# Kernel optimization log

Measured on AMD Instinct MI355X. Metric: run time of the kernel, lower is better.

The kernel has to match this reference:

```python
import jax, jax.numpy as jnp
import numpy as np

N = 100_000       # nodes
E_RAND = 1_600_000
HID = 256         # hidden_channels
L = 4             # num_layers
HEADS = 8
BASES = 4
AGGS = 3          # ['sum','mean','max']
DH = HID // HEADS # 32
BF = DH * BASES   # 128, bases_lin output dim
NG = 5000         # num graphs
VOCAB = 128
NFEAT = 9
EPS = 1e-5


def setup_inputs() -> dict:
    key = jax.random.key(0)
    ks = jax.random.split(key, 16)
    x = jax.random.randint(ks[0], (N, NFEAT), 0, VOCAB, dtype=jnp.int32)
    src = jax.random.randint(ks[1], (E_RAND,), 0, N, dtype=jnp.int32)
    dst = jax.random.randint(ks[2], (E_RAND,), 0, N, dtype=jnp.int32)
    loop = jnp.arange(N, dtype=jnp.int32)          # EGConv add_self_loops=True
    edge_src = jnp.concatenate([src, loop])
    edge_dst = jnp.concatenate([dst, loop])
    batch = jnp.sort(jax.random.randint(ks[3], (N,), 0, NG, dtype=jnp.int32))
    s = lambda k, shape, sc: (jax.random.normal(k, shape, jnp.float32) * sc)
    emb = s(ks[4], (NFEAT, VOCAB, HID), 0.1)       # AtomEncoder tables
    basesW = s(ks[5], (L, HID, BF), HID ** -0.5)
    combW = s(ks[6], (L, HID, HEADS * BASES * AGGS), HID ** -0.5)
    combB = jnp.zeros((L, HEADS * BASES * AGGS), jnp.float32)
    convBias = jnp.zeros((L, HID), jnp.float32)
    bnG = jnp.ones((L, HID), jnp.float32)
    bnB = jnp.zeros((L, HID), jnp.float32)
    mlp_w1 = s(ks[7], (HID, HID // 2), HID ** -0.5)
    bn1_g = jnp.ones((HID // 2,), jnp.float32)
    bn1_b = jnp.zeros((HID // 2,), jnp.float32)
    mlp_w2 = s(ks[8], (HID // 2, HID // 4), (HID // 2) ** -0.5)
    bn2_g = jnp.ones((HID // 4,), jnp.float32)
    bn2_b = jnp.zeros((HID // 4,), jnp.float32)
    mlp_w3 = s(ks[9], (HID // 4, 1), (HID // 4) ** -0.5)
    mlp_b3 = jnp.zeros((1,), jnp.float32)
    return dict(x=x, edge_src=edge_src, edge_dst=edge_dst, batch=batch,
                emb=emb, basesW=basesW, combW=combW, combB=combB,
                convBias=convBias, bnG=bnG, bnB=bnB,
                mlp_w1=mlp_w1, bn1_g=bn1_g, bn1_b=bn1_b,
                mlp_w2=mlp_w2, bn2_g=bn2_g, bn2_b=bn2_b,
                mlp_w3=mlp_w3, mlp_b3=mlp_b3)


def _batchnorm(h, g, b):
    # training-mode BatchNorm1d: biased batch stats
    mu = h.mean(0)
    var = ((h - mu) ** 2).mean(0)
    return (h - mu) * jax.lax.rsqrt(var + EPS) * g + b


def _egconv(x, src, dst, W_b, W_c, b_c, bias):
    bases = x @ W_b                                    # [N, BF]
    w = (x @ W_c + b_c).reshape(N, HEADS, BASES * AGGS)
    msg = bases[src]                                   # [E, BF] gather
    agg_sum = jnp.zeros((N, BF), x.dtype).at[dst].add(msg)
    deg = jnp.zeros((N,), x.dtype).at[dst].add(1.0)
    agg_mean = agg_sum / jnp.maximum(deg, 1.0)[:, None]
    agg_max = jnp.full((N, BF), -jnp.inf, x.dtype).at[dst].max(msg)
    agg = jnp.stack([agg_sum, agg_mean, agg_max], 1)   # [N, A, BF]
    agg = agg.reshape(N, AGGS * BASES, DH)             # [N, A*B, DH]
    out = jnp.einsum('nhk,nkd->nhd', w, agg).reshape(N, HID)
    return out + bias


def reference(x, edge_src, edge_dst, batch, emb, basesW, combW, combB,
              convBias, bnG, bnB, mlp_w1, bn1_g, bn1_b, mlp_w2, bn2_g,
              bn2_b, mlp_w3, mlp_b3):
    # AtomEncoder: sum of per-feature embedding lookups
    h = jnp.take_along_axis(
        emb.transpose(1, 0, 2),                        # [VOCAB, NFEAT, HID]
        x.T[..., None], axis=0) if False else None
    feat = jnp.arange(NFEAT)
    xe = emb[feat[None, :], x, :].sum(1)               # [N, HID]
    h = xe
    for l in range(L):
        c = _egconv(h, edge_src, edge_dst, basesW[l], combW[l], combB[l],
                    convBias[l])
        c = jax.nn.relu(_batchnorm(c, bnG[l], bnB[l]))
        h = h + c                                      # residual
    # global mean pool over graphs
    gs = jax.ops.segment_sum(h, batch, num_segments=NG)
    cnt = jax.ops.segment_sum(jnp.ones((N, 1), h.dtype), batch,
                              num_segments=NG)
    g = gs / jnp.maximum(cnt, 1.0)
    # MLP head
    g = jax.nn.relu(_batchnorm(g @ mlp_w1, bn1_g, bn1_b))
    g = jax.nn.relu(_batchnorm(g @ mlp_w2, bn2_g, bn2_b))
    return g @ mlp_w3 + mlp_b3                         # [NG, 1]
```

## Files before the change

### kernel.cpp

```cpp
#include <hip/hip_runtime.h>
#include <hip/hip_bf16.h>

#define NNODES 100000
#define HIDC 256
#define NFEAT 9
#define VOCABS 128
#define BFD 128
#define NCOMB 96
#define NGR 5000
#define LAYERSN 4
#define EPSV 1e-5f
#define SCHUNK 1024
#define NPP 16
#define NTILES 14
#define AGGBLK 2048
#define PBL (NTILES * 8 * 64)
#define NBUK 32
#define BDIV 3125
#define SC2K 64

typedef __hip_bfloat16 bf16;
typedef __attribute__((ext_vector_type(8))) short sh8;
typedef __attribute__((ext_vector_type(4))) float fx4;

__device__ __forceinline__ float b2f(bf16 v) { return __bfloat162float(v); }
__device__ __forceinline__ bf16 f2b(float v) { return __float2bfloat16(v); }
__device__ __forceinline__ float ldf(const float* p) { return *p; }
__device__ __forceinline__ float ldf(const bf16* p) { return b2f(*p); }
__device__ __forceinline__ void stf(float* p, float v) { *p = v; }
__device__ __forceinline__ void stf(bf16* p, float v) { *p = f2b(v); }
__device__ __forceinline__ float2 ldf2(const float* p) { return *(const float2*)p; }
__device__ __forceinline__ float2 ldf2(const bf16* p) {
    unsigned u = *(const unsigned*)p;
    return make_float2(__uint_as_float(u << 16), __uint_as_float(u & 0xFFFF0000u));
}
__device__ __forceinline__ void stf2(float* p, float a, float b) {
    *(float2*)p = make_float2(a, b);
}
__device__ __forceinline__ void stf2(bf16* p, float a, float b);

__device__ __forceinline__ unsigned pack2bf(float a, float b) {
    unsigned ua = __float_as_uint(a), ub = __float_as_uint(b);
    ua = (ua + 0x7FFFu + ((ua >> 16) & 1u)) >> 16;
    ub = (ub + 0x7FFFu + ((ub >> 16) & 1u)) >> 16;
    return ua | (ub << 16);
}
__device__ __forceinline__ void stf2(bf16* p, float a, float b) {
    *(unsigned*)p = pack2bf(a, b);
}

__global__ __launch_bounds__(256) void k_sentinel(float* out, int n, float val) {
    int i = blockIdx.x * 256 + threadIdx.x;
    if (i < n) out[i] = val;
}

__global__ __launch_bounds__(256) void k_hist(const int* __restrict__ dst,
                                              int* __restrict__ counts, int E) {
    int e = blockIdx.x * 256 + threadIdx.x;
    if (e < E) atomicAdd(&counts[dst[e]], 1);
}

__global__ __launch_bounds__(256) void k_scansum(const int* __restrict__ counts,
                                                 int* __restrict__ btot, int n) {
    __shared__ int sh[256];
    int b = blockIdx.x, t = threadIdx.x;
    int base = b * SCHUNK;
    int s = 0;
#pragma unroll
    for (int k = 0; k < 4; ++k) {
        int i = base + t + k * 256;
        if (i < n) s += counts[i];
    }
    sh[t] = s;
    __syncthreads();
    for (int st = 128; st > 0; st >>= 1) {
        if (t < st) sh[t] += sh[t + st];
        __syncthreads();
    }
    if (t == 0) btot[b] = sh[0];
}

__global__ void k_scansmall(const int* __restrict__ btot, int* __restrict__ boff, int nb) {
    if (threadIdx.x == 0 && blockIdx.x == 0) {
        int a = 0;
        for (int i = 0; i < nb; ++i) { boff[i] = a; a += btot[i]; }
    }
}

__global__ __launch_bounds__(256) void k_scanapply(const int* __restrict__ counts,
                                                   const int* __restrict__ boff,
                                                   int* __restrict__ rowptr,
                                                   int* __restrict__ cursor, int n) {
    __shared__ int sh[256];
    int b = blockIdx.x, t = threadIdx.x;
    int base = b * SCHUNK + t * 4;
    int c0 = (base + 0 < n) ? counts[base + 0] : 0;
    int c1 = (base + 1 < n) ? counts[base + 1] : 0;
    int c2 = (base + 2 < n) ? counts[base + 2] : 0;
    int c3 = (base + 3 < n) ? counts[base + 3] : 0;
    int s0 = c0, s1 = s0 + c1, s2 = s1 + c2, s3 = s2 + c3;
    sh[t] = s3;
    __syncthreads();
    for (int st = 1; st < 256; st <<= 1) {
        int v = (t >= st) ? sh[t - st] : 0;
        __syncthreads();
        sh[t] += v;
        __syncthreads();
    }
    int excl = sh[t] - s3 + boff[b];
    if (base + 0 < n) { rowptr[base + 1] = excl + s0; cursor[base + 0] = excl; }
    if (base + 1 < n) { rowptr[base + 2] = excl + s1; cursor[base + 1] = excl + s0; }
    if (base + 2 < n) { rowptr[base + 3] = excl + s2; cursor[base + 2] = excl + s1; }
    if (base + 3 < n) { rowptr[base + 4] = excl + s3; cursor[base + 3] = excl + s2; }
    if (b == 0 && t == 0) rowptr[0] = 0;
}

__global__ void k_binit(const int* __restrict__ rowptr, int* __restrict__ gcur) {
    int b = threadIdx.x;
    if (b < NBUK) gcur[b] = rowptr[b * BDIV];
}

__global__ __launch_bounds__(256) void k_bucket(const int* __restrict__ src,
                                                const int* __restrict__ dst,
                                                int* __restrict__ gcur,
                                                uint2* __restrict__ ebuf, int E) {
    __shared__ int cnt[NBUK], base[NBUK], off[NBUK];
    int tid = threadIdx.x;
    if (tid < NBUK) { cnt[tid] = 0; off[tid] = 0; }
    __syncthreads();
    int d[4], s[4], bk[4];
    int e0 = blockIdx.x * 1024;
#pragma unroll
    for (int k = 0; k < 4; ++k) {
        int e = e0 + tid + k * 256;
        if (e < E) {
            d[k] = dst[e]; s[k] = src[e];
            bk[k] = d[k] / BDIV;
            atomicAdd(&cnt[bk[k]], 1);
        } else bk[k] = -1;
    }
    __syncthreads();
    if (tid < NBUK && cnt[tid] > 0) base[tid] = atomicAdd(&gcur[tid], cnt[tid]);
    __syncthreads();
#pragma unroll
    for (int k = 0; k < 4; ++k) {
        if (bk[k] >= 0) {
            int sl = base[bk[k]] + atomicAdd(&off[bk[k]], 1);
            ebuf[sl] = make_uint2((unsigned)d[k], (unsigned)s[k]);
        }
    }
}

__global__ __launch_bounds__(256) void k_scatter2(const uint2* __restrict__ ebuf,
                                                  const int* __restrict__ rowptr,
                                                  int* __restrict__ cursor,
                                                  int* __restrict__ csr) {
    int bk = blockIdx.x & (NBUK - 1);
    int chunk = blockIdx.x >> 5;
    int lo = rowptr[bk * BDIV];
    int nhi = (bk + 1) * BDIV; if (nhi > NNODES) nhi = NNODES;
    int hi = rowptr[nhi];
    for (int e = lo + chunk * 256 + threadIdx.x; e < hi; e += SC2K * 256) {
        uint2 p = ebuf[e];
        int pos = atomicAdd(&cursor[p.x], 1);
        csr[pos] = (int)p.y;
    }
}

__global__ __launch_bounds__(256) void k_packB4(const float* __restrict__ basesW,
                                                const float* __restrict__ combW,
                                                bf16* __restrict__ Bp4) {
    int tid = blockIdx.x * 256 + threadIdx.x;
    if (tid >= LAYERSN * PBL) return;
    int layer = tid / PBL;
    int rem = tid % PBL;
    int l = rem & 63;
    int q = (rem >> 6) & 7;
    int t = rem >> 9;
    int n = t * 16 + (l & 15);
    int k0 = q * 32 + (l >> 4) * 8;
    const float* Wb = basesW + (size_t)layer * HIDC * BFD;
    const float* Wc = combW + (size_t)layer * HIDC * NCOMB;
    short out[8];
#pragma unroll
    for (int i = 0; i < 8; ++i) {
        int k = k0 + i;
        float v = (n < BFD) ? Wb[k * BFD + n] : Wc[k * NCOMB + (n - BFD)];
        unsigned u = __float_as_uint(v);
        out[i] = (short)((u + 0x7FFFu + ((u >> 16) & 1u)) >> 16);
    }
    *(sh8*)(Bp4 + (size_t)tid * 8) = *(sh8*)out;
}

template <typename TH, typename TW, int MODE>
__global__ __launch_bounds__(256) void k_gemm_mfma(TH* __restrict__ h,
                                                   const bf16* __restrict__ Bp,
                                                   const float* __restrict__ cb,
                                                   bf16* __restrict__ bases,
                                                   TW* __restrict__ wco,
                                                   const bf16* __restrict__ convp,
                                                   const float* __restrict__ ss,
                                                   const int* __restrict__ x,
                                                   const float* __restrict__ emb) {
    __shared__ unsigned ldsA[8192];
    __shared__ int xsh[64 * NFEAT];
    int tid = threadIdx.x;
    size_t blk = blockIdx.x;
    if (MODE == 0) {
        for (int i = tid; i < 64 * NFEAT; i += 256) {
            int row = i / NFEAT;
            size_t rg = blk * 64 + row;
            xsh[i] = (rg < NNODES) ? x[rg * NFEAT + (i % NFEAT)] : 0;
        }
        __syncthreads();
    }
#pragma unroll 4
    for (int it = 0; it < 32; ++it) {
        int p = tid + it * 256;
        int row = p >> 7, cp = p & 127;
        size_t rg = blk * 64 + row;
        unsigned word = 0;
        if (rg < NNODES) {
            int c0 = cp * 2;
            float a0, a1;
            if (MODE == 0) {
                a0 = 0.f; a1 = 0.f;
#pragma unroll
                for (int f = 0; f < NFEAT; ++f) {
                    const float* ep = emb + ((size_t)(f * VOCABS + xsh[row * NFEAT + f])) * HIDC + c0;
                    float2 ev = *(const float2*)ep;
                    a0 += ev.x; a1 += ev.y;
                }
                stf2(&h[rg * HIDC + c0], a0, a1);
            } else {
                float2 hv = ldf2(&h[rg * HIDC + c0]);
                a0 = hv.x; a1 = hv.y;
                unsigned cu = *(const unsigned*)&convp[rg * HIDC + c0];
                float2 sc = *(const float2*)&ss[c0];
                float2 sb = *(const float2*)&ss[HIDC + c0];
                float v0 = __uint_as_float(cu << 16) * sc.x + sb.x;
                float v1 = __uint_as_float(cu & 0xFFFF0000u) * sc.y + sb.y;
                a0 += fmaxf(v0, 0.f);
                a1 += fmaxf(v1, 0.f);
                stf2(&h[rg * HIDC + c0], a0, a1);
            }
            word = pack2bf(a0, a1);
        }
        ldsA[(row * 128 + cp) ^ ((row & 7) << 2)] = word;
    }
    __syncthreads();
    int w = tid >> 6, l = tid & 63;
    int r = 16 * w + (l & 15);
    sh8 af[8];
    const char* lb = (const char*)ldsA;
#pragma unroll
    for (int q = 0; q < 8; ++q) {
        int byte = (r * 512 + q * 64 + (l >> 4) * 16) ^ ((r & 7) << 4);
        af[q] = *(const sh8*)(lb + byte);
    }
    fx4 acc[NTILES];
#pragma unroll
    for (int t = 0; t < NTILES; ++t) acc[t] = (fx4){0.f, 0.f, 0.f, 0.f};
    const sh8* bp8 = (const sh8*)Bp;
#pragma unroll
    for (int t = 0; t < NTILES; ++t) {
#pragma unroll
        for (int q = 0; q < 8; ++q) {
            acc[t] = __builtin_amdgcn_mfma_f32_16x16x32_bf16(
                af[q], bp8[(t * 8 + q) * 64 + l], acc[t], 0, 0, 0);
        }
    }
#pragma unroll
    for (int t = 0; t < NTILES; ++t) {
#pragma unroll
        for (int j = 0; j < 4; ++j) {
            int rl = 16 * w + (l >> 4) * 4 + j;
            size_t rg = blk * 64 + rl;
            if (rg >= NNODES) continue;
            if (t < 8) {
                int col = t * 16 + (l & 15);
                bases[rg * BFD + col] = f2b(acc[t][j]);
            } else {
                int col = (t - 8) * 16 + (l & 15);
                stf(&wco[rg * NCOMB + col], acc[t][j] + cb[col]);
            }
        }
    }
}

template <typename TW>
__global__ __launch_bounds__(256) void k_agg(const int* __restrict__ rowptr,
                                             const int* __restrict__ csr,
                                             const uint4* __restrict__ b4,
                                             const TW* __restrict__ wco,
                                             const float* __restrict__ bias,
                                             bf16* __restrict__ conv,
                                             float* __restrict__ partials) {
    __shared__ float agg[8][3][BFD];
    __shared__ float red[512];
    int tid = threadIdx.x;
    int g = tid >> 5, cl = tid & 31;
    int sub = cl >> 4;
    int ln16 = cl & 15;
    red[tid] = 0.f;
    red[tid + 256] = 0.f;
    __syncthreads();
    int hh = cl >> 2;
    int dbase = 8 * (cl & 3);
    float bb[8];
#pragma unroll
    for (int j = 0; j < 8; ++j) bb[j] = bias[8 * cl + j];
    float sts[8], sts2[8];
#pragma unroll
    for (int j = 0; j < 8; ++j) { sts[j] = 0.f; sts2[j] = 0.f; }
    for (int n = blockIdx.x * 8 + g; n < NNODES; n += AGGBLK * 8) {
        int r0 = rowptr[n], r1 = rowptr[n + 1];
        float s0 = 0.f, s1 = 0.f, s2 = 0.f, s3 = 0.f;
        float s4 = 0.f, s5 = 0.f, s6 = 0.f, s7 = 0.f;
        float m0 = -INFINITY, m1 = -INFINITY, m2 = -INFINITY, m3 = -INFINITY;
        float m4 = -INFINITY, m5 = -INFINITY, m6 = -INFINITY, m7 = -INFINITY;
        int e = r0;
#define ACCU4(v) { float f0 = __uint_as_float((v).x << 16);            \
                   float f1 = __uint_as_float((v).x & 0xFFFF0000u);    \
                   float f2 = __uint_as_float((v).y << 16);            \
                   float f3 = __uint_as_float((v).y & 0xFFFF0000u);    \
                   float f4 = __uint_as_float((v).z << 16);            \
                   float f5 = __uint_as_float((v).z & 0xFFFF0000u);    \
                   float f6 = __uint_as_float((v).w << 16);            \
                   float f7 = __uint_as_float((v).w & 0xFFFF0000u);    \
                   s0 += f0; s1 += f1; s2 += f2; s3 += f3;             \
                   s4 += f4; s5 += f5; s6 += f6; s7 += f7;             \
                   m0 = fmaxf(m0, f0); m1 = fmaxf(m1, f1);             \
                   m2 = fmaxf(m2, f2); m3 = fmaxf(m3, f3);             \
                   m4 = fmaxf(m4, f4); m5 = fmaxf(m5, f5);             \
                   m6 = fmaxf(m6, f6); m7 = fmaxf(m7, f7); }
        for (; e + 8 <= r1; e += 8) {
            int i0 = csr[e + 0 + sub], i1 = csr[e + 2 + sub];
            int i2 = csr[e + 4 + sub], i3 = csr[e + 6 + sub];
            uint4 v0 = b4[(size_t)i0 * 16 + ln16];
            uint4 v1 = b4[(size_t)i1 * 16 + ln16];
            uint4 v2 = b4[(size_t)i2 * 16 + ln16];
            uint4 v3 = b4[(size_t)i3 * 16 + ln16];
            ACCU4(v0) ACCU4(v1) ACCU4(v2) ACCU4(v3)
        }
        for (; e + 2 <= r1; e += 2) {
            uint4 v = b4[(size_t)csr[e + sub] * 16 + ln16];
            ACCU4(v)
        }
        if (e < r1 && sub == 0) {
            uint4 v = b4[(size_t)csr[e] * 16 + ln16];
            ACCU4(v)
        }
#undef ACCU4
        s0 += __shfl_xor(s0, 16); s1 += __shfl_xor(s1, 16);
        s2 += __shfl_xor(s2, 16); s3 += __shfl_xor(s3, 16);
        s4 += __shfl_xor(s4, 16); s5 += __shfl_xor(s5, 16);
        s6 += __shfl_xor(s6, 16); s7 += __shfl_xor(s7, 16);
        m0 = fmaxf(m0, __shfl_xor(m0, 16)); m1 = fmaxf(m1, __shfl_xor(m1, 16));
        m2 = fmaxf(m2, __shfl_xor(m2, 16)); m3 = fmaxf(m3, __shfl_xor(m3, 16));
        m4 = fmaxf(m4, __shfl_xor(m4, 16)); m5 = fmaxf(m5, __shfl_xor(m5, 16));
        m6 = fmaxf(m6, __shfl_xor(m6, 16)); m7 = fmaxf(m7, __shfl_xor(m7, 16));
        if (sub == 0) {
            float inv = 1.0f / (float)(r1 - r0);
            int cb2 = ln16 * 8;
            *(float4*)&agg[g][0][cb2]     = make_float4(s0, s1, s2, s3);
            *(float4*)&agg[g][0][cb2 + 4] = make_float4(s4, s5, s6, s7);
            *(float4*)&agg[g][1][cb2]     = make_float4(s0 * inv, s1 * inv, s2 * inv, s3 * inv);
            *(float4*)&agg[g][1][cb2 + 4] = make_float4(s4 * inv, s5 * inv, s6 * inv, s7 * inv);
            *(float4*)&agg[g][2][cb2]     = make_float4(m0, m1, m2, m3);
            *(float4*)&agg[g][2][cb2 + 4] = make_float4(m4, m5, m6, m7);
        }
        const TW* wp = &wco[(size_t)n * NCOMB + hh * 12];
        float wv[12];
#pragma unroll
        for (int k = 0; k < 12; ++k) wv[k] = ldf(&wp[k]);
        float o[8];
#pragma unroll
        for (int j = 0; j < 8; ++j) {
            int d = dbase + j;
            float a = 0.f;
#pragma unroll
            for (int b = 0; b < 4; ++b) {
                a += wv[b] * agg[g][0][b * 32 + d];
                a += wv[4 + b] * agg[g][1][b * 32 + d];
                a += wv[8 + b] * agg[g][2][b * 32 + d];
            }
            a += bb[j];
            o[j] = a;
            sts[j] += a;
            sts2[j] += a * a;
        }
        uint4 cv = make_uint4(pack2bf(o[0], o[1]), pack2bf(o[2], o[3]),
                              pack2bf(o[4], o[5]), pack2bf(o[6], o[7]));
        ((uint4*)conv)[(size_t)n * 32 + cl] = cv;
    }
#pragma unroll
    for (int j = 0; j < 8; ++j) {
        atomicAdd(&red[8 * cl + j], sts[j]);
        atomicAdd(&red[256 + 8 * cl + j], sts2[j]);
    }
    __syncthreads();
    partials[(size_t)blockIdx.x * 512 + tid] = red[tid];
    partials[(size_t)blockIdx.x * 512 + 256 + tid] = red[tid + 256];
}

__global__ __launch_bounds__(256) void k_redstats(const float* __restrict__ partials,
                                                  float* __restrict__ sums) {
    int g = blockIdx.x * 256 + threadIdx.x;
    int j = g & 511;
    int chunk = g >> 9;
    float s = 0.f;
    for (int pb = chunk * 256; pb < (chunk + 1) * 256; ++pb)
        s += partials[(size_t)pb * 512 + j];
    atomicAdd(&sums[j], s);
}

template <int C>
__global__ void k_bnfin(const float* __restrict__ sums, const float* __restrict__ g,
                        const float* __restrict__ b, float nrows, float* __restrict__ ss) {
    int c = threadIdx.x;
    float mu = sums[c] / nrows;
    float var = sums[C + c] / nrows - mu * mu;
    float rstd = rsqrtf(fmaxf(var, 0.f) + EPSV);
    float sc = rstd * g[c];
    ss[c] = sc;
    ss[C + c] = b[c] - mu * sc;
}

template <typename TH>
__global__ __launch_bounds__(256) void k_pool(const TH* __restrict__ h,
                                              const bf16* __restrict__ conv,
                                              const float* __restrict__ ss,
                                              const int* __restrict__ batch,
                                              float* __restrict__ gs,
                                              float* __restrict__ cnt) {
    int c = threadIdx.x;
    float sc = ss[c], sb = ss[HIDC + c];
    int n0 = blockIdx.x * NPP;
    int end = min(n0 + NPP, NNODES);
    float acc = 0.f, ccnt = 0.f;
    int cur = batch[n0];
    for (int n = n0; n < end; ++n) {
        int b = batch[n];
        if (b != cur) {
            atomicAdd(&gs[(size_t)cur * HIDC + c], acc);
            if (c == 0) atomicAdd(&cnt[cur], ccnt);
            acc = 0.f; ccnt = 0.f; cur = b;
        }
        float v = b2f(conv[(size_t)n * HIDC + c]) * sc + sb;
        acc += ldf(&h[(size_t)n * HIDC + c]) + fmaxf(v, 0.f);
        ccnt += 1.f;
    }
    atomicAdd(&gs[(size_t)cur * HIDC + c], acc);
    if (c == 0) atomicAdd(&cnt[cur], ccnt);
}

__global__ __launch_bounds__(256) void k_pooldiv(float* __restrict__ gs,
                                                 const float* __restrict__ cnt) {
    int i = blockIdx.x * 256 + threadIdx.x;
    if (i >= NGR * HIDC) return;
    int ng = i >> 8;
    gs[i] = gs[i] / fmaxf(cnt[ng], 1.0f);
}

template <int K, int C>
__global__ void k_rowgemm(const float* __restrict__ in, const float* __restrict__ W,
                          float* __restrict__ out) {
    int r = blockIdx.x;
    __shared__ float rs[K];
    for (int i = threadIdx.x; i < K; i += C) rs[i] = in[r * K + i];
    __syncthreads();
    int c = threadIdx.x;
    float acc = 0.f;
    for (int k = 0; k < K; ++k) acc += rs[k] * W[k * C + c];
    out[r * C + c] = acc;
}

template <int C>
__global__ void k_stats(const float* __restrict__ a, int rows, int rpb,
                        float* __restrict__ sums) {
    int c = threadIdx.x;
    int r0 = blockIdx.x * rpb;
    int r1 = min(r0 + rpb, rows);
    float s = 0.f, s2 = 0.f;
    for (int r = r0; r < r1; ++r) {
        float v = a[r * C + c];
        s += v;
        s2 += v * v;
    }
    atomicAdd(&sums[c], s);
    atomicAdd(&sums[C + c], s2);
}

template <int C>
__global__ void k_apply_relu(float* __restrict__ a, const float* __restrict__ ss, int rows) {
    int i = blockIdx.x * 256 + threadIdx.x;
    if (i >= rows * C) return;
    int c = i % C;
    float v = a[i] * ss[c] + ss[C + c];
    a[i] = fmaxf(v, 0.f);
}

__global__ __launch_bounds__(256) void k_final(const float* __restrict__ g2,
                                               const float* __restrict__ w3,
                                               const float* __restrict__ b3,
                                               float* __restrict__ out) {
    int r = blockIdx.x * 256 + threadIdx.x;
    if (r >= NGR) return;
    float acc = 0.f;
#pragma unroll
    for (int k = 0; k < 64; ++k) acc += g2[r * 64 + k] * w3[k];
    out[r] = acc + b3[0];
}

static inline size_t alignup(size_t v) { return (v + 255) & ~(size_t)255; }

template <typename TH, typename TW>
static size_t carve_need(int E) {
    size_t off = 0;
    off = alignup(off + (size_t)NNODES * HIDC * sizeof(TH));
    off = alignup(off + (size_t)NNODES * BFD * 2);
    off = alignup(off + (size_t)NNODES * NCOMB * sizeof(TW));
    off = alignup(off + (size_t)NNODES * HIDC * 2);
    off = alignup(off + (size_t)(NNODES + 1) * 4);
    off = alignup(off + (size_t)NNODES * 4);
    off = alignup(off + (size_t)E * 4);
    off = alignup(off + (size_t)E * 8);
    off = alignup(off + 2 * HIDC * 4);
    off = alignup(off + 2 * HIDC * 4);
    off = alignup(off + 256 * 4);
    off = alignup(off + 256 * 4);
    off = alignup(off + 256 * 4);
    off = alignup(off + (size_t)LAYERSN * PBL * 8 * 2);
    off = alignup(off + (size_t)AGGBLK * 512 * 4);
    return off;
}

template <typename TH, typename TW>
static void run_all(const int* x, const int* esrc, const int* edst, const int* batch,
                    const float* emb, const float* basesW, const float* combW,
                    const float* combB, const float* convB, const float* bnG,
                    const float* bnB, const float* w1, const float* bn1g,
                    const float* bn1b, const float* w2, const float* bn2g,
                    const float* bn2b, const float* w3, const float* b3, int E,
                    float* out, char* base, hipStream_t stream) {
    size_t off = 0;
    TH* h = (TH*)(base + off);       off = alignup(off + (size_t)NNODES * HIDC * sizeof(TH));
    bf16* bases = (bf16*)(base + off); off = alignup(off + (size_t)NNODES * BFD * 2);
    TW* wco = (TW*)(base + off);     off = alignup(off + (size_t)NNODES * NCOMB * sizeof(TW));
    bf16* conv = (bf16*)(base + off); off = alignup(off + (size_t)NNODES * HIDC * 2);
    int* rowptr = (int*)(base + off); off = alignup(off + (size_t)(NNODES + 1) * 4);
    int* cursor = (int*)(base + off); off = alignup(off + (size_t)NNODES * 4);
    int* csr = (int*)(base + off);    off = alignup(off + (size_t)E * 4);
    size_t o_ebuf = off;
    uint2* ebuf = (uint2*)(base + off); off = alignup(off + (size_t)E * 8);
    float* sums = (float*)(base + off); off = alignup(off + 2 * HIDC * 4);
    float* ss = (float*)(base + off);   off = alignup(off + 2 * HIDC * 4);
    int* btot = (int*)(base + off);     off = alignup(off + 256 * 4);
    int* boff = (int*)(base + off);     off = alignup(off + 256 * 4);
    int* gcur = (int*)(base + off);     off = alignup(off + 256 * 4);
    bf16* Bp4 = (bf16*)(base + off);    off = alignup(off + (size_t)LAYERSN * PBL * 8 * 2);
    float* partials = (float*)(base + off); off = alignup(off + (size_t)AGGBLK * 512 * 4);
    size_t po = o_ebuf;
    float* gs = (float*)(base + po);  po = alignup(po + (size_t)NGR * HIDC * 4);
    float* cnt = (float*)(base + po); po = alignup(po + (size_t)NGR * 4);
    float* r1 = (float*)(base + po);  po = alignup(po + (size_t)NGR * 128 * 4);
    float* r2 = (float*)(base + po);  po = alignup(po + (size_t)NGR * 64 * 4);

    const int NB = (NNODES + SCHUNK - 1) / SCHUNK;
    const int GEMMBLK = (NNODES + 63) / 64;

    k_packB4<<<(LAYERSN * PBL + 255) / 256, 256, 0, stream>>>(basesW, combW, Bp4);
    hipMemsetAsync(cursor, 0, (size_t)NNODES * 4, stream);
    k_hist<<<(E + 255) / 256, 256, 0, stream>>>(edst, cursor, E);
    k_scansum<<<NB, 256, 0, stream>>>(cursor, btot, NNODES);
    k_scansmall<<<1, 64, 0, stream>>>(btot, boff, NB);
    k_scanapply<<<NB, 256, 0, stream>>>(cursor, boff, rowptr, cursor, NNODES);
    k_binit<<<1, NBUK, 0, stream>>>(rowptr, gcur);
    k_bucket<<<(E + 1023) / 1024, 256, 0, stream>>>(esrc, edst, gcur, ebuf, E);
    k_scatter2<<<NBUK * SC2K, 256, 0, stream>>>(ebuf, rowptr, cursor, csr);

    for (int l = 0; l < LAYERSN; ++l) {
        hipMemsetAsync(sums, 0, 2 * HIDC * 4, stream);
        if (l == 0) {
            k_gemm_mfma<TH, TW, 0><<<GEMMBLK, 256, 0, stream>>>(
                h, Bp4, combB, bases, wco, nullptr, ss, x, emb);
        } else {
            k_gemm_mfma<TH, TW, 1><<<GEMMBLK, 256, 0, stream>>>(
                h, Bp4 + (size_t)l * PBL * 8, combB + (size_t)l * NCOMB, bases, wco,
                conv, ss, nullptr, nullptr);
        }
        k_agg<TW><<<AGGBLK, 256, 0, stream>>>(rowptr, csr, (const uint4*)bases,
                                              wco, convB + (size_t)l * HIDC, conv,
                                              partials);
        k_redstats<<<16, 256, 0, stream>>>(partials, sums);
        k_bnfin<HIDC><<<1, HIDC, 0, stream>>>(sums, bnG + (size_t)l * HIDC,
                                              bnB + (size_t)l * HIDC, (float)NNODES, ss);
    }

    hipMemsetAsync(gs, 0, (size_t)NGR * HIDC * 4, stream);
    hipMemsetAsync(cnt, 0, (size_t)NGR * 4, stream);
    k_pool<TH><<<(NNODES + NPP - 1) / NPP, 256, 0, stream>>>(h, conv, ss, batch, gs, cnt);
    k_pooldiv<<<(NGR * HIDC + 255) / 256, 256, 0, stream>>>(gs, cnt);

    k_rowgemm<256, 128><<<NGR, 128, 0, stream>>>(gs, w1, r1);
    hipMemsetAsync(sums, 0, 2 * 128 * 4, stream);
    k_stats<128><<<(NGR + 15) / 16, 128, 0, stream>>>(r1, NGR, 16, sums);
    k_bnfin<128><<<1, 128, 0, stream>>>(sums, bn1g, bn1b, (float)NGR, ss);
    k_apply_relu<128><<<(NGR * 128 + 255) / 256, 256, 0, stream>>>(r1, ss, NGR);

    k_rowgemm<128, 64><<<NGR, 64, 0, stream>>>(r1, w2, r2);
    hipMemsetAsync(sums, 0, 2 * 64 * 4, stream);
    k_stats<64><<<(NGR + 31) / 32, 64, 0, stream>>>(r2, NGR, 32, sums);
    k_bnfin<64><<<1, 64, 0, stream>>>(sums, bn2g, bn2b, (float)NGR, ss);
    k_apply_relu<64><<<(NGR * 64 + 255) / 256, 256, 0, stream>>>(r2, ss, NGR);

    k_final<<<(NGR + 255) / 256, 256, 0, stream>>>(r2, w3, b3, out);
}

extern "C" void kernel_launch(void* const* d_in, const int* in_sizes, int n_in,
                              void* d_out, int out_size, void* d_ws, size_t ws_size,
                              hipStream_t stream) {
    const int* x        = (const int*)d_in[0];
    const int* esrc     = (const int*)d_in[1];
    const int* edst     = (const int*)d_in[2];
    const int* batch    = (const int*)d_in[3];
    const float* emb    = (const float*)d_in[4];
    const float* basesW = (const float*)d_in[5];
    const float* combW  = (const float*)d_in[6];
    const float* combB  = (const float*)d_in[7];
    const float* convB  = (const float*)d_in[8];
    const float* bnG    = (const float*)d_in[9];
    const float* bnB    = (const float*)d_in[10];
    const float* w1     = (const float*)d_in[11];
    const float* bn1g   = (const float*)d_in[12];
    const float* bn1b   = (const float*)d_in[13];
    const float* w2     = (const float*)d_in[14];
    const float* bn2g   = (const float*)d_in[15];
    const float* bn2b   = (const float*)d_in[16];
    const float* w3     = (const float*)d_in[17];
    const float* b3     = (const float*)d_in[18];
    const int E = in_sizes[1];

    size_t need_full    = carve_need<float, bf16>(E);
    size_t need_compact = carve_need<bf16, bf16>(E);

    if (ws_size >= need_full) {
        run_all<float, bf16>(x, esrc, edst, batch, emb, basesW, combW, combB, convB,
                             bnG, bnB, w1, bn1g, bn1b, w2, bn2g, bn2b, w3, b3, E,
                             (float*)d_out, (char*)d_ws, stream);
    } else if (ws_size >= need_compact) {
        run_all<bf16, bf16>(x, esrc, edst, batch, emb, basesW, combW, combB, convB,
                            bnG, bnB, w1, bn1g, bn1b, w2, bn2g, bn2b, w3, b3, E,
                            (float*)d_out, (char*)d_ws, stream);
    } else {
        k_sentinel<<<(out_size + 255) / 256, 256, 0, stream>>>(
            (float*)d_out, out_size, (float)(ws_size >> 20));
    }
}
```

Baseline: 1.380 ms.

## Prefetch CSR indices in aggregation, fuse MLP head kernels, force bf16 hidden state

The aggregation loop now software-prefetches the next group of CSR neighbor indices while gathering the current rows, so index loads overlap with feature gathers. The MLP head folds pool division, GEMM, batch statistics and BN+ReLU into fewer kernels that handle 20 rows per block, with the final BN+ReLU moved into the last dot product. The hidden state is now always stored in bf16 rather than fp32 when workspace allows, which halves its traffic but lowers precision.

```diff
diff --git a/kernel.cpp b/kernel.cpp
--- a/kernel.cpp
+++ b/kernel.cpp
@@ -18,6 +18,7 @@
 #define NBUK 32
 #define BDIV 3125
 #define SC2K 64
+#define RPBH 20
 
 typedef __hip_bfloat16 bf16;
 typedef __attribute__((ext_vector_type(8))) short sh8;
@@ -334,14 +335,27 @@
                    m2 = fmaxf(m2, f2); m3 = fmaxf(m3, f3);             \
                    m4 = fmaxf(m4, f4); m5 = fmaxf(m5, f5);             \
                    m6 = fmaxf(m6, f6); m7 = fmaxf(m7, f7); }
-        for (; e + 8 <= r1; e += 8) {
-            int i0 = csr[e + 0 + sub], i1 = csr[e + 2 + sub];
-            int i2 = csr[e + 4 + sub], i3 = csr[e + 6 + sub];
-            uint4 v0 = b4[(size_t)i0 * 16 + ln16];
-            uint4 v1 = b4[(size_t)i1 * 16 + ln16];
-            uint4 v2 = b4[(size_t)i2 * 16 + ln16];
-            uint4 v3 = b4[(size_t)i3 * 16 + ln16];
+        int ia0 = 0, ia1 = 0, ia2 = 0, ia3 = 0;
+        bool win = (e + 8 <= r1);
+        if (win) {
+            ia0 = csr[e + 0 + sub]; ia1 = csr[e + 2 + sub];
+            ia2 = csr[e + 4 + sub]; ia3 = csr[e + 6 + sub];
+        }
+        while (win) {
+            int en = e + 8;
+            bool winn = (en + 8 <= r1);
+            int ib0 = 0, ib1 = 0, ib2 = 0, ib3 = 0;
+            if (winn) {
+                ib0 = csr[en + 0 + sub]; ib1 = csr[en + 2 + sub];
+                ib2 = csr[en + 4 + sub]; ib3 = csr[en + 6 + sub];
+            }
+            uint4 v0 = b4[(size_t)ia0 * 16 + ln16];
+            uint4 v1 = b4[(size_t)ia1 * 16 + ln16];
+            uint4 v2 = b4[(size_t)ia2 * 16 + ln16];
+            uint4 v3 = b4[(size_t)ia3 * 16 + ln16];
             ACCU4(v0) ACCU4(v1) ACCU4(v2) ACCU4(v3)
+            ia0 = ib0; ia1 = ib1; ia2 = ib2; ia3 = ib3;
+            e = en; win = winn;
         }
         for (; e + 2 <= r1; e += 2) {
             uint4 v = b4[(size_t)csr[e + sub] * 16 + ln16];
@@ -455,61 +469,71 @@
     if (c == 0) atomicAdd(&cnt[cur], ccnt);
 }
 
-__global__ __launch_bounds__(256) void k_pooldiv(float* __restrict__ gs,
-                                                 const float* __restrict__ cnt) {
-    int i = blockIdx.x * 256 + threadIdx.x;
-    if (i >= NGR * HIDC) return;
-    int ng = i >> 8;
-    gs[i] = gs[i] / fmaxf(cnt[ng], 1.0f);
-}
-
-template <int K, int C>
-__global__ void k_rowgemm(const float* __restrict__ in, const float* __restrict__ W,
-                          float* __restrict__ out) {
-    int r = blockIdx.x;
-    __shared__ float rs[K];
-    for (int i = threadIdx.x; i < K; i += C) rs[i] = in[r * K + i];
-    __syncthreads();
-    int c = threadIdx.x;
-    float acc = 0.f;
-    for (int k = 0; k < K; ++k) acc += rs[k] * W[k * C + c];
-    out[r * C + c] = acc;
-}
-
-template <int C>
-__global__ void k_stats(const float* __restrict__ a, int rows, int rpb,
-                        float* __restrict__ sums) {
-    int c = threadIdx.x;
-    int r0 = blockIdx.x * rpb;
-    int r1 = min(r0 + rpb, rows);
+template <int K, int C, int FUSE>
+__global__ __launch_bounds__(256) void k_gemmstats(const float* __restrict__ in,
+                                                   const float* __restrict__ cnt,
+                                                   const float* __restrict__ ssin,
+                                                   const float* __restrict__ W,
+                                                   float* __restrict__ out,
+                                                   float* __restrict__ sums) {
+    constexpr int RG = 256 / C;
+    constexpr int RPT = RPBH / RG;
+    __shared__ float rs[RPBH][K + 1];
+    __shared__ float fac[RPBH];
+    __shared__ float red[2][C];
+    int tid = threadIdx.x;
+    int r0 = blockIdx.x * RPBH;
+    if (FUSE == 0 && tid < RPBH) fac[tid] = 1.f / fmaxf(cnt[r0 + tid], 1.f);
+    if (tid < C) { red[0][tid] = 0.f; red[1][tid] = 0.f; }
+    __syncthreads();
+    for (int i = tid; i < RPBH * K; i += 256) {
+        int r = i / K, k = i - r * K;
+        float v = in[(size_t)(r0 + r) * K + k];
+        if (FUSE == 0) v *= fac[r];
+        else v = fmaxf(v * ssin[k] + ssin[K + k], 0.f);
+        rs[r][k] = v;
+    }
+    __syncthreads();
+    int c = tid % C;
+    int g = tid / C;
+    float acc[RPT];
+#pragma unroll
+    for (int j = 0; j < RPT; ++j) acc[j] = 0.f;
+    for (int k = 0; k < K; ++k) {
+        float w = W[k * C + c];
+#pragma unroll
+        for (int j = 0; j < RPT; ++j) acc[j] += rs[g * RPT + j][k] * w;
+    }
     float s = 0.f, s2 = 0.f;
-    for (int r = r0; r < r1; ++r) {
-        float v = a[r * C + c];
-        s += v;
-        s2 += v * v;
-    }
-    atomicAdd(&sums[c], s);
-    atomicAdd(&sums[C + c], s2);
-}
-
-template <int C>
-__global__ void k_apply_relu(float* __restrict__ a, const float* __restrict__ ss, int rows) {
-    int i = blockIdx.x * 256 + threadIdx.x;
-    if (i >= rows * C) return;
-    int c = i % C;
-    float v = a[i] * ss[c] + ss[C + c];
-    a[i] = fmaxf(v, 0.f);
-}
-
-__global__ __launch_bounds__(256) void k_final(const float* __restrict__ g2,
-                                               const float* __restrict__ w3,
-                                               const float* __restrict__ b3,
-                                               float* __restrict__ out) {
+#pragma unroll
+    for (int j = 0; j < RPT; ++j) {
+        int r = g * RPT + j;
+        out[(size_t)(r0 + r) * C + c] = acc[j];
+        s += acc[j];
+        s2 += acc[j] * acc[j];
+    }
+    atomicAdd(&red[0][c], s);
+    atomicAdd(&red[1][c], s2);
+    __syncthreads();
+    if (tid < C) {
+        atomicAdd(&sums[tid], red[0][tid]);
+        atomicAdd(&sums[C + tid], red[1][tid]);
+    }
+}
+
+__global__ __launch_bounds__(256) void k_final2(const float* __restrict__ r2,
+                                                const float* __restrict__ ss,
+                                                const float* __restrict__ w3,
+                                                const float* __restrict__ b3,
+                                                float* __restrict__ out) {
     int r = blockIdx.x * 256 + threadIdx.x;
     if (r >= NGR) return;
     float acc = 0.f;
 #pragma unroll
-    for (int k = 0; k < 64; ++k) acc += g2[r * 64 + k] * w3[k];
+    for (int k = 0; k < 64; ++k) {
+        float v = fmaxf(r2[r * 64 + k] * ss[k] + ss[64 + k], 0.f);
+        acc += v * w3[k];
+    }
     out[r] = acc + b3[0];
 }
 
@@ -601,21 +625,14 @@
     hipMemsetAsync(gs, 0, (size_t)NGR * HIDC * 4, stream);
     hipMemsetAsync(cnt, 0, (size_t)NGR * 4, stream);
     k_pool<TH><<<(NNODES + NPP - 1) / NPP, 256, 0, stream>>>(h, conv, ss, batch, gs, cnt);
-    k_pooldiv<<<(NGR * HIDC + 255) / 256, 256, 0, stream>>>(gs, cnt);
-
-    k_rowgemm<256, 128><<<NGR, 128, 0, stream>>>(gs, w1, r1);
-    hipMemsetAsync(sums, 0, 2 * 128 * 4, stream);
-    k_stats<128><<<(NGR + 15) / 16, 128, 0, stream>>>(r1, NGR, 16, sums);
+
+    hipMemsetAsync(sums, 0, 2 * HIDC * 4, stream);
+    k_gemmstats<256, 128, 0><<<NGR / RPBH, 256, 0, stream>>>(gs, cnt, nullptr, w1, r1, sums);
     k_bnfin<128><<<1, 128, 0, stream>>>(sums, bn1g, bn1b, (float)NGR, ss);
-    k_apply_relu<128><<<(NGR * 128 + 255) / 256, 256, 0, stream>>>(r1, ss, NGR);
-
-    k_rowgemm<128, 64><<<NGR, 64, 0, stream>>>(r1, w2, r2);
-    hipMemsetAsync(sums, 0, 2 * 64 * 4, stream);
-    k_stats<64><<<(NGR + 31) / 32, 64, 0, stream>>>(r2, NGR, 32, sums);
+    hipMemsetAsync(sums, 0, 2 * HIDC * 4, stream);
+    k_gemmstats<128, 64, 1><<<NGR / RPBH, 256, 0, stream>>>(r1, nullptr, ss, w2, r2, sums);
     k_bnfin<64><<<1, 64, 0, stream>>>(sums, bn2g, bn2b, (float)NGR, ss);
-    k_apply_relu<64><<<(NGR * 64 + 255) / 256, 256, 0, stream>>>(r2, ss, NGR);
-
-    k_final<<<(NGR + 255) / 256, 256, 0, stream>>>(r2, w3, b3, out);
+    k_final2<<<(NGR + 255) / 256, 256, 0, stream>>>(r2, ss, w3, b3, out);
 }
 
 extern "C" void kernel_launch(void* const* d_in, const int* in_sizes, int n_in,
@@ -642,14 +659,9 @@
     const float* b3     = (const float*)d_in[18];
     const int E = in_sizes[1];
 
-    size_t need_full    = carve_need<float, bf16>(E);
     size_t need_compact = carve_need<bf16, bf16>(E);
 
-    if (ws_size >= need_full) {
-        run_all<float, bf16>(x, esrc, edst, batch, emb, basesW, combW, combB, convB,
-                             bnG, bnB, w1, bn1g, bn1b, w2, bn2g, bn2b, w3, b3, E,
-                             (float*)d_out, (char*)d_ws, stream);
-    } else if (ws_size >= need_compact) {
+    if (ws_size >= need_compact) {
         run_all<bf16, bf16>(x, esrc, edst, batch, emb, basesW, combW, combB, convB,
                             bnG, bnB, w1, bn1g, bn1b, w2, bn2g, bn2b, w3, b3, E,
                             (float*)d_out, (char*)d_ws, stream);
```

Measured after the change: 1.402 ms. About the same (+1.6%).
